# Kernel optimization log

Measured on AMD Instinct MI355X. Metric: run time of the kernel, lower is better.

Reference implementation:

```python
import jax, jax.numpy as jnp
import numpy as np

N = 100000  # nodes
E = 1600000  # edges


def gcn_conv(x, W, b, src, dst, n_nodes):
    """PyG-style GCNConv: add self-loops, symmetric norm, linear, scatter-add, bias."""
    h = x @ W  # [N, F_out]
    loop = jnp.arange(n_nodes, dtype=src.dtype)
    s = jnp.concatenate([src, loop])  # source nodes (messages flow src -> dst)
    d = jnp.concatenate([dst, loop])
    deg = jax.ops.segment_sum(jnp.ones_like(d, dtype=h.dtype), d, num_segments=n_nodes)
    dinv = jnp.where(deg > 0, jax.lax.rsqrt(deg), 0.0)
    norm = dinv[s] * dinv[d]  # [E+N]
    msgs = h[s] * norm[:, None]  # [E+N, F_out] -- dominant memory traffic
    out = jax.ops.segment_sum(msgs, d, num_segments=n_nodes)
    return out + b


def setup_inputs() -> dict:
    key = jax.random.key(0)
    k1, k2, k3, k4 = jax.random.split(key, 4)
    x = jax.random.normal(k1, (N, 128), dtype=jnp.float32)
    edge_index = jax.random.randint(k2, (2, E), 0, N, dtype=jnp.int32)
    W1 = jax.random.normal(k3, (128, 64), dtype=jnp.float32) * (1.0 / np.sqrt(128))
    b1 = jnp.zeros((64,), dtype=jnp.float32)
    W2 = jax.random.normal(k4, (64, 16), dtype=jnp.float32) * (1.0 / np.sqrt(64))
    b2 = jnp.zeros((16,), dtype=jnp.float32)
    return {"x": x, "edge_index": edge_index, "W1": W1, "b1": b1, "W2": W2, "b2": b2}


def reference(x, edge_index, W1, b1, W2, b2):
    src, dst = edge_index[0], edge_index[1]
    h = gcn_conv(x, W1, b1, src, dst, N)
    h = jax.nn.leaky_relu(h, negative_slope=0.2)
    # dropout is identity in eval mode
    h = gcn_conv(h, W2, b2, src, dst, N)
    return jax.nn.log_softmax(h, axis=-1)
```

## Files before the change

### kernel.cpp

```cpp
#include <hip/hip_runtime.h>
#include <math.h>


#define CHUNK 4096
#define BSHIFT 8
#define BMASK 255
#define CAP 4864
#define CAPP (CAP + 40)

typedef __bf16 bf16x8 __attribute__((ext_vector_type(8)));
typedef float f32x4 __attribute__((ext_vector_type(4)));

__device__ __forceinline__ unsigned f2b(float f) {
  unsigned u = __float_as_uint(f);
  return (u + 0x7FFF + ((u >> 16) & 1)) >> 16;
}

struct f2 { float x, y; };
__device__ __forceinline__ void addu(f2& a, unsigned u) {
  a.x += __uint_as_float(u << 16);
  a.y += __uint_as_float(u);
}
__device__ __forceinline__ void addu4(f2* a, uint4 g) {
  addu(a[0], g.x); addu(a[1], g.y); addu(a[2], g.z); addu(a[3], g.w);
}

__global__ void binit_kernel(int* __restrict__ gbcursor, int nbc,
                             unsigned* __restrict__ h1s, unsigned* __restrict__ t,
                             int n) {
  int b = blockIdx.x * 256 + threadIdx.x;
  if (b < nbc) gbcursor[b] = b * CAP;
  if (blockIdx.x == 0) {
    if (threadIdx.x < 32) h1s[(size_t)n * 32 + threadIdx.x] = 0u;
    else if (threadIdx.x < 40) t[(size_t)n * 8 + (threadIdx.x - 32)] = 0u;
  }
}

__global__ __launch_bounds__(256) void scatterA_kernel(const int* __restrict__ src,
                                                       const int* __restrict__ dst,
                                                       int E, int nbc,
                                                       int* __restrict__ gbcursor,
                                                       int* __restrict__ tmp) {
  __shared__ int hist[512];
  __shared__ int segcur[512];
  int tid = threadIdx.x;
  int estart = blockIdx.x * CHUNK;
  int eend = min(E, estart + CHUNK);
  hist[tid] = 0;
  hist[tid + 256] = 0;
  __syncthreads();
  for (int i = estart + tid; i < eend; i += 256)
    atomicAdd(&hist[dst[i] >> BSHIFT], 1);
  __syncthreads();
  for (int bb = tid; bb < nbc; bb += 256) {
    int c = hist[bb];
    segcur[bb] = c ? atomicAdd(&gbcursor[bb], c) : 0;
  }
  __syncthreads();
  for (int i = estart + tid; i < eend; i += 256) {
    int d = dst[i];
    int b = d >> BSHIFT;
    int pos = atomicAdd(&segcur[b], 1);
    if (pos < (b + 1) * CAP)
      tmp[pos] = (src[i] << BSHIFT) | (d & BMASK);
  }
}

__global__ __launch_bounds__(256) void degcnt_kernel(const int* __restrict__ tmp,
                                                     const int* __restrict__ gbcursor,
                                                     int* __restrict__ degs,
                                                     float* __restrict__ dinv, int n) {
  __shared__ int nh[256];
  int b = blockIdx.x, tid = threadIdx.x;
  nh[tid] = 0;
  __syncthreads();
  int base = b * CAP;
  int count = min(gbcursor[b] - base, CAP);
  for (int i = tid; i < count; i += 256) atomicAdd(&nh[tmp[base + i] & BMASK], 1);
  __syncthreads();
  int v = (b << BSHIFT) + tid;
  if (v < n) {
    degs[v] = nh[tid];
    dinv[v] = rsqrtf((float)(nh[tid] + 1));
  }
}

__global__ __launch_bounds__(256, 4) void gemm1_kernel(const float* __restrict__ x,
                                                       const float* __restrict__ W1,
                                                       const float* __restrict__ dinv,
                                                       unsigned* __restrict__ h1s, int n) {
  __shared__ unsigned lds_u[64 * 68 * 2];
  unsigned* xs = lds_u;
  unsigned* wt = lds_u + 64 * 68;
  int tid = threadIdx.x;
  int vb = blockIdx.x * 64;
  int nrows = min(64, n - vb);

  const float4* xg = (const float4*)(x + (size_t)vb * 128);
#pragma unroll
  for (int it = 0; it < 8; ++it) {
    int idx = it * 256 + tid;
    int r = idx >> 5, c2 = idx & 31;
    float4 vv = make_float4(0.f, 0.f, 0.f, 0.f);
    if (r < nrows) vv = xg[idx];
    xs[r * 68 + c2 * 2] = (f2b(vv.y) << 16) | f2b(vv.x);
    xs[r * 68 + c2 * 2 + 1] = (f2b(vv.w) << 16) | f2b(vv.z);
  }
  unsigned short* wt16 = (unsigned short*)wt;
  const float4* wg = (const float4*)W1;
#pragma unroll
  for (int it = 0; it < 8; ++it) {
    int idx = it * 256 + tid;
    int k = idx >> 4, n0 = (idx & 15) * 4;
    float4 wv = wg[idx];
    wt16[(n0 + 0) * 136 + k] = (unsigned short)f2b(wv.x);
    wt16[(n0 + 1) * 136 + k] = (unsigned short)f2b(wv.y);
    wt16[(n0 + 2) * 136 + k] = (unsigned short)f2b(wv.z);
    wt16[(n0 + 3) * 136 + k] = (unsigned short)f2b(wv.w);
  }
  __syncthreads();

  int lane = tid & 63, wid = tid >> 6;
  int m16 = lane & 15, quad = lane >> 4;
  const unsigned* xp = xs + (wid * 16 + m16) * 68 + quad * 4;
  const unsigned* wp = wt + m16 * 68 + quad * 4;
  f32x4 acc[4] = {};
#pragma unroll
  for (int ks = 0; ks < 4; ++ks) {
    bf16x8 a = *(const bf16x8*)(xp + ks * 16);
#pragma unroll
    for (int nt = 0; nt < 4; ++nt) {
      bf16x8 b = *(const bf16x8*)(wp + nt * 16 * 68 + ks * 16);
      acc[nt] = __builtin_amdgcn_mfma_f32_16x16x32_bf16(a, b, acc[nt], 0, 0, 0);
    }
  }
  int rbase = vb + wid * 16 + quad * 4;
  float dvv[4];
#pragma unroll
  for (int reg = 0; reg < 4; ++reg) {
    int row = rbase + reg;
    dvv[reg] = (row < n) ? dinv[row] : 0.f;
  }
  unsigned short* h16 = (unsigned short*)h1s;
#pragma unroll
  for (int nt = 0; nt < 4; ++nt) {
    int col = nt * 16 + m16;
#pragma unroll
    for (int reg = 0; reg < 4; ++reg) {
      int row = rbase + reg;
      if (row < n)
        h16[(size_t)row * 64 + col] = (unsigned short)f2b(dvv[reg] * acc[nt][reg]);
    }
  }
}

template <int NQ>
__device__ __forceinline__ void gatherTier1(const uint4* __restrict__ h1s4,
                                            const int* lcsr, int rs, int e1,
                                            int e, int c, int n, f2* a0) {
  int cv0[NQ], cv1[NQ];
#pragma unroll
  for (int q = 0; q < NQ; ++q) {
    cv0[q] = lcsr[rs + q * 8 + e];
    cv1[q] = lcsr[rs + q * 8 + 4 + e];
  }
  uint4 g[2 * NQ];
#pragma unroll
  for (int q = 0; q < NQ; ++q) {
    int k0 = rs + q * 8 + e, k1 = k0 + 4;
    int s0 = (k0 < e1) ? cv0[q] : n;
    int s1 = (k1 < e1) ? cv1[q] : n;
    g[2 * q] = h1s4[(size_t)s0 * 8 + c];
    g[2 * q + 1] = h1s4[(size_t)s1 * 8 + c];
  }
#pragma unroll
  for (int k = 0; k < 2 * NQ; ++k) addu4(a0, g[k]);
}

__global__ __launch_bounds__(1024) void agg1_fused_kernel(
    const int* __restrict__ tmp, const int* __restrict__ gbcursor,
    const uint4* __restrict__ h1s4, const float* __restrict__ dinv,
    const float* __restrict__ b1, const float* __restrict__ W2,
    const int* __restrict__ degs, int* __restrict__ row_start,
    int* __restrict__ csr, unsigned* __restrict__ t, int n) {
  __shared__ int lcsr[CAPP];
  __shared__ int nh[256];
  __shared__ int rs_s[256];
  __shared__ int lcur[256];
  __shared__ float W2s[64 * 17];
  __shared__ float b1s[64];
  __shared__ float a_s[16][2][64];
  int b = blockIdx.x, tid = threadIdx.x;
  int base = b * CAP;
  int count = min(gbcursor[b] - base, CAP);

  if (tid < 256) {
    int v = (b << BSHIFT) + tid;
    int d = (v < n) ? degs[v] : 0;
    nh[tid] = d;
    rs_s[tid] = d;
  }
  W2s[(tid >> 4) * 17 + (tid & 15)] = W2[tid];
  if (tid < 64) b1s[tid] = b1[tid];
  __syncthreads();
  for (int off = 1; off < 256; off <<= 1) {
    int a = 0;
    if (tid < 256) { a = rs_s[tid]; if (tid >= off) a += rs_s[tid - off]; }
    __syncthreads();
    if (tid < 256) rs_s[tid] = a;
    __syncthreads();
  }
  if (tid < 256) {
    int e0 = rs_s[tid] - nh[tid];
    lcur[tid] = e0;
    rs_s[tid] = e0;
    int v = (b << BSHIFT) + tid;
    if (v < n) row_start[v] = base + e0;
  }
  __syncthreads();
  for (int i = tid; i < count; i += 1024) {
    int val = tmp[base + i];
    int pos = atomicAdd(&lcur[val & BMASK], 1);
    lcsr[pos] = val >> BSHIFT;
  }
  __syncthreads();
  for (int i = tid; i < count; i += 1024) csr[base + i] = lcsr[i];

  int wave = tid >> 6, lane = tid & 63;
  int half = lane >> 5, sub = lane & 31;
  int e = sub >> 3, c = sub & 7;
  int j = sub & 15, grp = (sub >> 4) & 1;

#pragma unroll 1
  for (int it = 0; it < 8; ++it) {
    int nl = wave * 16 + it * 2 + half;
    int v = (b << BSHIFT) + nl;
    bool valid = (v < n);
    int rs = rs_s[nl];
    int deg = nh[nl];
    int e1 = rs + deg;
    float dv = valid ? dinv[valid ? v : 0] : 0.f;

    f2 a0[4];
#pragma unroll
    for (int k = 0; k < 4; ++k) a0[k] = {0.f, 0.f};
    {
      int s = (valid && sub < 8) ? v : n;
      addu4(a0, h1s4[(size_t)s * 8 + c]);
    }
    int dm = max(deg, __shfl_xor(deg, 32, 64));
    int start;
    if (dm <= 16) {
      gatherTier1<2>(h1s4, lcsr, rs, e1, e, c, n, a0);
      start = 16;
    } else if (dm <= 24) {
      gatherTier1<3>(h1s4, lcsr, rs, e1, e, c, n, a0);
      start = 24;
    } else {
      gatherTier1<4>(h1s4, lcsr, rs, e1, e, c, n, a0);
      start = 32;
    }
    int i = rs + start;
    while (__any(i < e1)) {
      int i0 = i + e, i1 = i + 4 + e;
      int s0v = lcsr[i0];
      int s1v = lcsr[i1];
      int s0 = (i0 < e1) ? s0v : n;
      int s1 = (i1 < e1) ? s1v : n;
      addu4(a0, h1s4[(size_t)s0 * 8 + c]);
      addu4(a0, h1s4[(size_t)s1 * 8 + c]);
      i += 8;
    }
#pragma unroll
    for (int m = 8; m <= 16; m <<= 1) {
#pragma unroll
      for (int k = 0; k < 4; ++k) {
        a0[k].x += __shfl_xor(a0[k].x, m, 64);
        a0[k].y += __shfl_xor(a0[k].y, m, 64);
      }
    }
    if (sub < 8) {
#pragma unroll
      for (int k = 0; k < 4; ++k) {
        float z0 = fmaf(dv, a0[k].x, b1s[8 * sub + 2 * k]);
        float z1 = fmaf(dv, a0[k].y, b1s[8 * sub + 2 * k + 1]);
        a_s[wave][half][8 * sub + 2 * k] = fmaxf(z0, 0.2f * z0);
        a_s[wave][half][8 * sub + 2 * k + 1] = fmaxf(z1, 0.2f * z1);
      }
    }
    float p = 0.f;
#pragma unroll
    for (int q = 0; q < 16; ++q) {
      int f = grp * 16 + q;
      p = fmaf(a_s[wave][half][f], W2s[f * 17 + j], p);
    }
#pragma unroll
    for (int q = 0; q < 16; ++q) {
      int f = 32 + grp * 16 + q;
      p = fmaf(a_s[wave][half][f], W2s[f * 17 + j], p);
    }
    p += __shfl_xor(p, 16, 64);
    float pv = dv * p;
    float po = __shfl_xor(pv, 1, 64);
    if (valid && sub < 16 && !(sub & 1))
      t[(size_t)v * 8 + (sub >> 1)] = (f2b(po) << 16) | f2b(pv);
  }
}

__global__ __launch_bounds__(256) void agg2_kernel(const uint4* __restrict__ t4,
                                                   const float* __restrict__ dinv,
                                                   const int* __restrict__ row_start,
                                                   const int* __restrict__ degs,
                                                   const int* __restrict__ csr,
                                                   const float* __restrict__ b2,
                                                   float* __restrict__ out, int n) {
  int idx = blockIdx.x * 256 + threadIdx.x;
  int v = idx >> 4;
  if (v >= n) return;
  int sub = threadIdx.x & 15;
  int e = sub >> 1, c = sub & 1;
  float dv = dinv[v];
  int rs = row_start[v], e1 = rs + degs[v];
  f2 A0[4];
#pragma unroll
  for (int k = 0; k < 4; ++k) A0[k] = {0.f, 0.f};
  {
    int s = (e == 0) ? v : n;
    addu4(A0, t4[(size_t)s * 2 + c]);
  }
  int cv[4];
#pragma unroll
  for (int q = 0; q < 4; ++q) cv[q] = csr[rs + q * 8 + e];
  uint4 g[4];
#pragma unroll
  for (int q = 0; q < 4; ++q) {
    int k = rs + q * 8 + e;
    int s = (k < e1) ? cv[q] : n;
    g[q] = t4[(size_t)s * 2 + c];
  }
#pragma unroll
  for (int k = 0; k < 4; ++k) addu4(A0, g[k]);
  int i = rs + 32;
  while (i < e1) {
    int i0 = i + e;
    int sv = csr[i0];
    int s = (i0 < e1) ? sv : n;
    addu4(A0, t4[(size_t)s * 2 + c]);
    i += 8;
  }
#pragma unroll
  for (int m = 2; m <= 8; m <<= 1) {
#pragma unroll
    for (int k = 0; k < 4; ++k) {
      A0[k].x += __shfl_xor(A0[k].x, m, 64);
      A0[k].y += __shfl_xor(A0[k].y, m, 64);
    }
  }
  float4 bb0 = ((const float4*)b2)[c * 2];
  float4 bb1 = ((const float4*)b2)[c * 2 + 1];
  float z[8];
  z[0] = fmaf(dv, A0[0].x, bb0.x); z[1] = fmaf(dv, A0[0].y, bb0.y);
  z[2] = fmaf(dv, A0[1].x, bb0.z); z[3] = fmaf(dv, A0[1].y, bb0.w);
  z[4] = fmaf(dv, A0[2].x, bb1.x); z[5] = fmaf(dv, A0[2].y, bb1.y);
  z[6] = fmaf(dv, A0[3].x, bb1.z); z[7] = fmaf(dv, A0[3].y, bb1.w);
  float mx = z[0];
#pragma unroll
  for (int q = 1; q < 8; ++q) mx = fmaxf(mx, z[q]);
  mx = fmaxf(mx, __shfl_xor(mx, 1, 64));
  float ss = 0.f;
#pragma unroll
  for (int q = 0; q < 8; ++q) ss += expf(z[q] - mx);
  ss += __shfl_xor(ss, 1, 64);
  float lg = mx + logf(ss);
  if (e == 0) {
    float4 r0 = make_float4(z[0] - lg, z[1] - lg, z[2] - lg, z[3] - lg);
    float4 r1 = make_float4(z[4] - lg, z[5] - lg, z[6] - lg, z[7] - lg);
    float4* o = (float4*)out + (size_t)v * 4 + c * 2;
    o[0] = r0;
    o[1] = r1;
  }
}

extern "C" void kernel_launch(void* const* d_in, const int* in_sizes, int n_in,
                              void* d_out, int out_size, void* d_ws, size_t ws_size,
                              hipStream_t stream) {
  const float* x = (const float*)d_in[0];
  const int* edge_index = (const int*)d_in[1];
  const float* W1 = (const float*)d_in[2];
  const float* b1 = (const float*)d_in[3];
  const float* W2 = (const float*)d_in[4];
  const float* b2 = (const float*)d_in[5];
  float* out = (float*)d_out;

  int N_ = in_sizes[0] / 128;
  int E_ = in_sizes[1] / 2;
  const int* src = edge_index;
  const int* dst = edge_index + E_;
  int NBc = (N_ + BMASK) >> BSHIFT;

  char* ws = (char*)d_ws;
  size_t off = 0;
  auto take = [&](size_t bytes) {
    void* p = ws + off;
    off += (bytes + 255) & ~(size_t)255;
    return p;
  };
  unsigned* h1s = (unsigned*)take(((size_t)N_ + 1) * 32 * 4);
  unsigned* t = (unsigned*)take(((size_t)N_ + 1) * 8 * 4);
  int* tmp = (int*)take((size_t)NBc * CAP * 4);
  int* csr = (int*)take(((size_t)NBc * CAP + 64) * 4);
  float* dinv = (float*)take((size_t)N_ * 4);
  int* degs = (int*)take((size_t)N_ * 4);
  int* row_start = (int*)take((size_t)N_ * 4);
  int* gbcursor = (int*)take((size_t)NBc * 4);
  (void)ws_size;

  binit_kernel<<<(NBc + 255) / 256, 256, 0, stream>>>(gbcursor, NBc, h1s, t, N_);
  scatterA_kernel<<<(E_ + CHUNK - 1) / CHUNK, 256, 0, stream>>>(src, dst, E_, NBc,
                                                                gbcursor, tmp);
  degcnt_kernel<<<NBc, 256, 0, stream>>>(tmp, gbcursor, degs, dinv, N_);
  gemm1_kernel<<<(N_ + 63) / 64, 256, 0, stream>>>(x, W1, dinv, h1s, N_);
  agg1_fused_kernel<<<NBc, 1024, 0, stream>>>(tmp, gbcursor, (const uint4*)h1s,
                                              dinv, b1, W2, degs, row_start, csr,
                                              t, N_);
  agg2_kernel<<<(N_ * 16 + 255) / 256, 256, 0, stream>>>((const uint4*)t, dinv,
                                                         row_start, degs, csr,
                                                         b2, out, N_);
}
```

Before: 203.4 us.

## Split layer-2 GEMM out of agg1 into separate MFMA bf16 kernel

Removes the per-node 64x16 W2 projection from the fused aggregation kernel. agg1 now writes bf16 leaky-relu activations to a new h2in buffer, and a new gemm2 kernel computes them times W2 with MFMA 16x16x32 bf16 instructions before scaling by dinv. This takes the LDS traffic and scalar FMA loop out of the latency-bound gather kernel and may improve its occupancy. The cost is an extra launch and a write plus re-read of a 64-wide bf16 intermediate of about 12.8MB, and W2 is now rounded to bf16.

New measurement: 209.6 us. +3.1%, slower.

```diff
diff --git a/kernel.cpp b/kernel.cpp
--- a/kernel.cpp
+++ b/kernel.cpp
@@ -180,16 +180,14 @@
 __global__ __launch_bounds__(1024) void agg1_fused_kernel(
     const int* __restrict__ tmp, const int* __restrict__ gbcursor,
     const uint4* __restrict__ h1s4, const float* __restrict__ dinv,
-    const float* __restrict__ b1, const float* __restrict__ W2,
-    const int* __restrict__ degs, int* __restrict__ row_start,
-    int* __restrict__ csr, unsigned* __restrict__ t, int n) {
+    const float* __restrict__ b1, const int* __restrict__ degs,
+    int* __restrict__ row_start, int* __restrict__ csr,
+    unsigned* __restrict__ h2in, int n) {
   __shared__ int lcsr[CAPP];
   __shared__ int nh[256];
   __shared__ int rs_s[256];
   __shared__ int lcur[256];
-  __shared__ float W2s[64 * 17];
   __shared__ float b1s[64];
-  __shared__ float a_s[16][2][64];
   int b = blockIdx.x, tid = threadIdx.x;
   int base = b * CAP;
   int count = min(gbcursor[b] - base, CAP);
@@ -200,7 +198,6 @@
     nh[tid] = d;
     rs_s[tid] = d;
   }
-  W2s[(tid >> 4) * 17 + (tid & 15)] = W2[tid];
   if (tid < 64) b1s[tid] = b1[tid];
   __syncthreads();
   for (int off = 1; off < 256; off <<= 1) {
@@ -229,7 +226,6 @@
   int wave = tid >> 6, lane = tid & 63;
   int half = lane >> 5, sub = lane & 31;
   int e = sub >> 3, c = sub & 7;
-  int j = sub & 15, grp = (sub >> 4) & 1;
 
 #pragma unroll 1
   for (int it = 0; it < 8; ++it) {
@@ -279,31 +275,57 @@
         a0[k].y += __shfl_xor(a0[k].y, m, 64);
       }
     }
-    if (sub < 8) {
+    if (valid && sub < 8) {
+      float z[8];
 #pragma unroll
       for (int k = 0; k < 4; ++k) {
         float z0 = fmaf(dv, a0[k].x, b1s[8 * sub + 2 * k]);
         float z1 = fmaf(dv, a0[k].y, b1s[8 * sub + 2 * k + 1]);
-        a_s[wave][half][8 * sub + 2 * k] = fmaxf(z0, 0.2f * z0);
-        a_s[wave][half][8 * sub + 2 * k + 1] = fmaxf(z1, 0.2f * z1);
+        z[2 * k] = fmaxf(z0, 0.2f * z0);
+        z[2 * k + 1] = fmaxf(z1, 0.2f * z1);
       }
-    }
-    float p = 0.f;
-#pragma unroll
-    for (int q = 0; q < 16; ++q) {
-      int f = grp * 16 + q;
-      p = fmaf(a_s[wave][half][f], W2s[f * 17 + j], p);
-    }
-#pragma unroll
-    for (int q = 0; q < 16; ++q) {
-      int f = 32 + grp * 16 + q;
-      p = fmaf(a_s[wave][half][f], W2s[f * 17 + j], p);
-    }
-    p += __shfl_xor(p, 16, 64);
-    float pv = dv * p;
-    float po = __shfl_xor(pv, 1, 64);
-    if (valid && sub < 16 && !(sub & 1))
-      t[(size_t)v * 8 + (sub >> 1)] = (f2b(po) << 16) | f2b(pv);
+      uint4 o;
+      o.x = (f2b(z[1]) << 16) | f2b(z[0]);
+      o.y = (f2b(z[3]) << 16) | f2b(z[2]);
+      o.z = (f2b(z[5]) << 16) | f2b(z[4]);
+      o.w = (f2b(z[7]) << 16) | f2b(z[6]);
+      ((uint4*)h2in)[(size_t)v * 8 + sub] = o;
+    }
+  }
+}
+
+__global__ __launch_bounds__(256) void gemm2_kernel(const uint4* __restrict__ h2in4,
+                                                    const float* __restrict__ W2,
+                                                    const float* __restrict__ dinv,
+                                                    unsigned* __restrict__ t, int n) {
+  int tid = threadIdx.x;
+  int lane = tid & 63, wid = tid >> 6;
+  int m16 = lane & 15, quad = lane >> 4;
+  union { bf16x8 v; unsigned short s[8]; } bu0, bu1;
+#pragma unroll
+  for (int j = 0; j < 8; ++j) {
+    bu0.s[j] = (unsigned short)f2b(W2[(quad * 8 + j) * 16 + m16]);
+    bu1.s[j] = (unsigned short)f2b(W2[(32 + quad * 8 + j) * 16 + m16]);
+  }
+#pragma unroll 1
+  for (int pass = 0; pass < 4; ++pass) {
+    int rt = blockIdx.x * 256 + pass * 64 + wid * 16;
+    int row_a = rt + m16;
+    int ra = (row_a < n) ? row_a : 0;
+    uint4 av0 = h2in4[(size_t)ra * 8 + quad];
+    uint4 av1 = h2in4[(size_t)ra * 8 + 4 + quad];
+    f32x4 acc = {};
+    acc = __builtin_amdgcn_mfma_f32_16x16x32_bf16(*(const bf16x8*)&av0, bu0.v, acc, 0, 0, 0);
+    acc = __builtin_amdgcn_mfma_f32_16x16x32_bf16(*(const bf16x8*)&av1, bu1.v, acc, 0, 0, 0);
+#pragma unroll
+    for (int reg = 0; reg < 4; ++reg) {
+      int row = rt + quad * 4 + reg;
+      float dv = (row < n) ? dinv[row] : 0.f;
+      float val = dv * acc[reg];
+      float other = __shfl_xor(val, 1, 64);
+      if (!(m16 & 1) && row < n)
+        t[(size_t)row * 8 + (m16 >> 1)] = (f2b(other) << 16) | f2b(val);
+    }
   }
 }
 
@@ -406,6 +428,7 @@
     return p;
   };
   unsigned* h1s = (unsigned*)take(((size_t)N_ + 1) * 32 * 4);
+  unsigned* h2in = (unsigned*)take(((size_t)N_ + 256) * 32 * 4);
   unsigned* t = (unsigned*)take(((size_t)N_ + 1) * 8 * 4);
   int* tmp = (int*)take((size_t)NBc * CAP * 4);
   int* csr = (int*)take(((size_t)NBc * CAP + 64) * 4);
@@ -421,8 +444,10 @@
   degcnt_kernel<<<NBc, 256, 0, stream>>>(tmp, gbcursor, degs, dinv, N_);
   gemm1_kernel<<<(N_ + 63) / 64, 256, 0, stream>>>(x, W1, dinv, h1s, N_);
   agg1_fused_kernel<<<NBc, 1024, 0, stream>>>(tmp, gbcursor, (const uint4*)h1s,
-                                              dinv, b1, W2, degs, row_start, csr,
-                                              t, N_);
+                                              dinv, b1, degs, row_start, csr,
+                                              h2in, N_);
+  gemm2_kernel<<<(N_ + 255) / 256, 256, 0, stream>>>((const uint4*)h2in, W2, dinv,
+                                                     t, N_);
   agg2_kernel<<<(N_ * 16 + 255) / 256, 256, 0, stream>>>((const uint4*)t, dinv,
                                                          row_start, degs, csr,
                                                          b2, out, N_);
```

## Merge edge bucketing and GEMM1 into one launch, scale h1 after degree count

Applied to the files above, without the earlier changes.

Edge bucketing and the first dense GEMM now run as two block roles inside a single kernel, so they overlap. The GEMM writes unscaled fp32 output to a workspace region that aliases csr and t, and a combined degree-count kernel applies dinv and converts to bf16. Buckets are widened from 256 to 512 nodes, which doubles per-block work in the aggregation kernel and halves the bucket count. This adds an extra fp32 round trip of h1 through memory and changes occupancy and per-bucket capacity.

Measured after the change: 204.9 us. No clear change (+0.8%).

```diff
diff --git a/kernel.cpp b/kernel.cpp
--- a/kernel.cpp
+++ b/kernel.cpp
@@ -2,10 +2,10 @@
 #include <math.h>
 
 
-#define CHUNK 4096
-#define BSHIFT 8
-#define BMASK 255
-#define CAP 4864
+#define CHUNK 8192
+#define BSHIFT 9
+#define BMASK 511
+#define CAP 9216
 #define CAPP (CAP + 40)
 
 typedef __bf16 bf16x8 __attribute__((ext_vector_type(8)));
@@ -26,130 +26,133 @@
 }
 
 __global__ void binit_kernel(int* __restrict__ gbcursor, int nbc,
-                             unsigned* __restrict__ h1s, unsigned* __restrict__ t,
-                             int n) {
+                             unsigned* __restrict__ h1s, int n) {
   int b = blockIdx.x * 256 + threadIdx.x;
   if (b < nbc) gbcursor[b] = b * CAP;
-  if (blockIdx.x == 0) {
-    if (threadIdx.x < 32) h1s[(size_t)n * 32 + threadIdx.x] = 0u;
-    else if (threadIdx.x < 40) t[(size_t)n * 8 + (threadIdx.x - 32)] = 0u;
-  }
-}
-
-__global__ __launch_bounds__(256) void scatterA_kernel(const int* __restrict__ src,
-                                                       const int* __restrict__ dst,
-                                                       int E, int nbc,
-                                                       int* __restrict__ gbcursor,
-                                                       int* __restrict__ tmp) {
-  __shared__ int hist[512];
-  __shared__ int segcur[512];
+  if (blockIdx.x == 0 && threadIdx.x < 32) h1s[(size_t)n * 32 + threadIdx.x] = 0u;
+}
+
+__global__ __launch_bounds__(256, 4) void combo_kernel(
+    const int* __restrict__ src, const int* __restrict__ dst, int E, int nbc,
+    int nSc, int* __restrict__ gbcursor, int* __restrict__ tmp,
+    const float* __restrict__ x, const float* __restrict__ W1,
+    float* __restrict__ h1u, int n) {
+  __shared__ unsigned shbuf[64 * 68 * 2];
   int tid = threadIdx.x;
-  int estart = blockIdx.x * CHUNK;
-  int eend = min(E, estart + CHUNK);
-  hist[tid] = 0;
-  hist[tid + 256] = 0;
-  __syncthreads();
-  for (int i = estart + tid; i < eend; i += 256)
-    atomicAdd(&hist[dst[i] >> BSHIFT], 1);
-  __syncthreads();
-  for (int bb = tid; bb < nbc; bb += 256) {
-    int c = hist[bb];
-    segcur[bb] = c ? atomicAdd(&gbcursor[bb], c) : 0;
-  }
-  __syncthreads();
-  for (int i = estart + tid; i < eend; i += 256) {
-    int d = dst[i];
-    int b = d >> BSHIFT;
-    int pos = atomicAdd(&segcur[b], 1);
-    if (pos < (b + 1) * CAP)
-      tmp[pos] = (src[i] << BSHIFT) | (d & BMASK);
-  }
-}
-
-__global__ __launch_bounds__(256) void degcnt_kernel(const int* __restrict__ tmp,
-                                                     const int* __restrict__ gbcursor,
-                                                     int* __restrict__ degs,
-                                                     float* __restrict__ dinv, int n) {
-  __shared__ int nh[256];
+
+  if ((int)blockIdx.x < nSc) {
+    int* hist = (int*)shbuf;
+    int* segcur = hist + 256;
+    int estart = blockIdx.x * CHUNK;
+    int eend = min(E, estart + CHUNK);
+    hist[tid] = 0;
+    __syncthreads();
+    for (int i = estart + tid; i < eend; i += 256)
+      atomicAdd(&hist[dst[i] >> BSHIFT], 1);
+    __syncthreads();
+    if (tid < nbc) {
+      int c = hist[tid];
+      segcur[tid] = c ? atomicAdd(&gbcursor[tid], c) : 0;
+    }
+    __syncthreads();
+    for (int i = estart + tid; i < eend; i += 256) {
+      int d = dst[i];
+      int b = d >> BSHIFT;
+      int pos = atomicAdd(&segcur[b], 1);
+      if (pos < (b + 1) * CAP)
+        tmp[pos] = (src[i] << BSHIFT) | (d & BMASK);
+    }
+  } else {
+    unsigned* xs = shbuf;
+    unsigned* wt = shbuf + 64 * 68;
+    int vb = ((int)blockIdx.x - nSc) * 64;
+    int nrows = min(64, n - vb);
+
+    const float4* xg = (const float4*)(x + (size_t)vb * 128);
+#pragma unroll
+    for (int it = 0; it < 8; ++it) {
+      int idx = it * 256 + tid;
+      int r = idx >> 5, c2 = idx & 31;
+      float4 vv = make_float4(0.f, 0.f, 0.f, 0.f);
+      if (r < nrows) vv = xg[idx];
+      xs[r * 68 + c2 * 2] = (f2b(vv.y) << 16) | f2b(vv.x);
+      xs[r * 68 + c2 * 2 + 1] = (f2b(vv.w) << 16) | f2b(vv.z);
+    }
+    unsigned short* wt16 = (unsigned short*)wt;
+    const float4* wg = (const float4*)W1;
+#pragma unroll
+    for (int it = 0; it < 8; ++it) {
+      int idx = it * 256 + tid;
+      int k = idx >> 4, n0 = (idx & 15) * 4;
+      float4 wv = wg[idx];
+      wt16[(n0 + 0) * 136 + k] = (unsigned short)f2b(wv.x);
+      wt16[(n0 + 1) * 136 + k] = (unsigned short)f2b(wv.y);
+      wt16[(n0 + 2) * 136 + k] = (unsigned short)f2b(wv.z);
+      wt16[(n0 + 3) * 136 + k] = (unsigned short)f2b(wv.w);
+    }
+    __syncthreads();
+
+    int lane = tid & 63, wid = tid >> 6;
+    int m16 = lane & 15, quad = lane >> 4;
+    const unsigned* xp = xs + (wid * 16 + m16) * 68 + quad * 4;
+    const unsigned* wp = wt + m16 * 68 + quad * 4;
+    f32x4 acc[4] = {};
+#pragma unroll
+    for (int ks = 0; ks < 4; ++ks) {
+      bf16x8 a = *(const bf16x8*)(xp + ks * 16);
+#pragma unroll
+      for (int nt = 0; nt < 4; ++nt) {
+        bf16x8 b = *(const bf16x8*)(wp + nt * 16 * 68 + ks * 16);
+        acc[nt] = __builtin_amdgcn_mfma_f32_16x16x32_bf16(a, b, acc[nt], 0, 0, 0);
+      }
+    }
+    int rbase = vb + wid * 16 + quad * 4;
+#pragma unroll
+    for (int nt = 0; nt < 4; ++nt) {
+      int col = nt * 16 + m16;
+#pragma unroll
+      for (int reg = 0; reg < 4; ++reg) {
+        int row = rbase + reg;
+        if (row < n) h1u[(size_t)row * 64 + col] = acc[nt][reg];
+      }
+    }
+  }
+}
+
+__global__ __launch_bounds__(512) void degcnt_scale_kernel(
+    const int* __restrict__ tmp, const int* __restrict__ gbcursor,
+    const float4* __restrict__ h1u4, int* __restrict__ degs,
+    float* __restrict__ dinv, unsigned* __restrict__ h1s, int n) {
+  __shared__ int nh[512];
+  __shared__ float dl[512];
   int b = blockIdx.x, tid = threadIdx.x;
   nh[tid] = 0;
   __syncthreads();
   int base = b * CAP;
   int count = min(gbcursor[b] - base, CAP);
-  for (int i = tid; i < count; i += 256) atomicAdd(&nh[tmp[base + i] & BMASK], 1);
-  __syncthreads();
-  int v = (b << BSHIFT) + tid;
-  if (v < n) {
-    degs[v] = nh[tid];
-    dinv[v] = rsqrtf((float)(nh[tid] + 1));
-  }
-}
-
-__global__ __launch_bounds__(256, 4) void gemm1_kernel(const float* __restrict__ x,
-                                                       const float* __restrict__ W1,
-                                                       const float* __restrict__ dinv,
-                                                       unsigned* __restrict__ h1s, int n) {
-  __shared__ unsigned lds_u[64 * 68 * 2];
-  unsigned* xs = lds_u;
-  unsigned* wt = lds_u + 64 * 68;
-  int tid = threadIdx.x;
-  int vb = blockIdx.x * 64;
-  int nrows = min(64, n - vb);
-
-  const float4* xg = (const float4*)(x + (size_t)vb * 128);
-#pragma unroll
-  for (int it = 0; it < 8; ++it) {
-    int idx = it * 256 + tid;
-    int r = idx >> 5, c2 = idx & 31;
-    float4 vv = make_float4(0.f, 0.f, 0.f, 0.f);
-    if (r < nrows) vv = xg[idx];
-    xs[r * 68 + c2 * 2] = (f2b(vv.y) << 16) | f2b(vv.x);
-    xs[r * 68 + c2 * 2 + 1] = (f2b(vv.w) << 16) | f2b(vv.z);
-  }
-  unsigned short* wt16 = (unsigned short*)wt;
-  const float4* wg = (const float4*)W1;
-#pragma unroll
-  for (int it = 0; it < 8; ++it) {
-    int idx = it * 256 + tid;
-    int k = idx >> 4, n0 = (idx & 15) * 4;
-    float4 wv = wg[idx];
-    wt16[(n0 + 0) * 136 + k] = (unsigned short)f2b(wv.x);
-    wt16[(n0 + 1) * 136 + k] = (unsigned short)f2b(wv.y);
-    wt16[(n0 + 2) * 136 + k] = (unsigned short)f2b(wv.z);
-    wt16[(n0 + 3) * 136 + k] = (unsigned short)f2b(wv.w);
-  }
-  __syncthreads();
-
-  int lane = tid & 63, wid = tid >> 6;
-  int m16 = lane & 15, quad = lane >> 4;
-  const unsigned* xp = xs + (wid * 16 + m16) * 68 + quad * 4;
-  const unsigned* wp = wt + m16 * 68 + quad * 4;
-  f32x4 acc[4] = {};
-#pragma unroll
-  for (int ks = 0; ks < 4; ++ks) {
-    bf16x8 a = *(const bf16x8*)(xp + ks * 16);
-#pragma unroll
-    for (int nt = 0; nt < 4; ++nt) {
-      bf16x8 b = *(const bf16x8*)(wp + nt * 16 * 68 + ks * 16);
-      acc[nt] = __builtin_amdgcn_mfma_f32_16x16x32_bf16(a, b, acc[nt], 0, 0, 0);
-    }
-  }
-  int rbase = vb + wid * 16 + quad * 4;
-  float dvv[4];
-#pragma unroll
-  for (int reg = 0; reg < 4; ++reg) {
-    int row = rbase + reg;
-    dvv[reg] = (row < n) ? dinv[row] : 0.f;
-  }
-  unsigned short* h16 = (unsigned short*)h1s;
-#pragma unroll
-  for (int nt = 0; nt < 4; ++nt) {
-    int col = nt * 16 + m16;
-#pragma unroll
-    for (int reg = 0; reg < 4; ++reg) {
-      int row = rbase + reg;
-      if (row < n)
-        h16[(size_t)row * 64 + col] = (unsigned short)f2b(dvv[reg] * acc[nt][reg]);
+  for (int i = tid; i < count; i += 512) atomicAdd(&nh[tmp[base + i] & BMASK], 1);
+  __syncthreads();
+  int v0 = (b << BSHIFT) + tid;
+  float dvv = rsqrtf((float)(nh[tid] + 1));
+  dl[tid] = dvv;
+  if (v0 < n) {
+    degs[v0] = nh[tid];
+    dinv[v0] = dvv;
+  }
+  __syncthreads();
+  uint2* h1s2 = (uint2*)h1s;
+#pragma unroll 4
+  for (int it = 0; it < 16; ++it) {
+    int idx = it * 512 + tid;
+    int rl = idx >> 4, q = idx & 15;
+    int v = (b << BSHIFT) + rl;
+    if (v < n) {
+      float4 vv = h1u4[(size_t)v * 16 + q];
+      float dv = dl[rl];
+      uint2 o;
+      o.x = (f2b(dv * vv.y) << 16) | f2b(dv * vv.x);
+      o.y = (f2b(dv * vv.w) << 16) | f2b(dv * vv.z);
+      h1s2[(size_t)v * 16 + q] = o;
     }
   }
 }
@@ -184,9 +187,9 @@
     const int* __restrict__ degs, int* __restrict__ row_start,
     int* __restrict__ csr, unsigned* __restrict__ t, int n) {
   __shared__ int lcsr[CAPP];
-  __shared__ int nh[256];
-  __shared__ int rs_s[256];
-  __shared__ int lcur[256];
+  __shared__ int nh[512];
+  __shared__ int rs_s[512];
+  __shared__ int lcur[512];
   __shared__ float W2s[64 * 17];
   __shared__ float b1s[64];
   __shared__ float a_s[16][2][64];
@@ -194,7 +197,7 @@
   int base = b * CAP;
   int count = min(gbcursor[b] - base, CAP);
 
-  if (tid < 256) {
+  if (tid < 512) {
     int v = (b << BSHIFT) + tid;
     int d = (v < n) ? degs[v] : 0;
     nh[tid] = d;
@@ -202,15 +205,17 @@
   }
   W2s[(tid >> 4) * 17 + (tid & 15)] = W2[tid];
   if (tid < 64) b1s[tid] = b1[tid];
-  __syncthreads();
-  for (int off = 1; off < 256; off <<= 1) {
+  if (b == 0 && tid >= 64 && tid < 72)
+    t[(size_t)n * 8 + (tid - 64)] = 0u;
+  __syncthreads();
+  for (int off = 1; off < 512; off <<= 1) {
     int a = 0;
-    if (tid < 256) { a = rs_s[tid]; if (tid >= off) a += rs_s[tid - off]; }
-    __syncthreads();
-    if (tid < 256) rs_s[tid] = a;
-    __syncthreads();
-  }
-  if (tid < 256) {
+    if (tid < 512) { a = rs_s[tid]; if (tid >= off) a += rs_s[tid - off]; }
+    __syncthreads();
+    if (tid < 512) rs_s[tid] = a;
+    __syncthreads();
+  }
+  if (tid < 512) {
     int e0 = rs_s[tid] - nh[tid];
     lcur[tid] = e0;
     rs_s[tid] = e0;
@@ -232,8 +237,8 @@
   int j = sub & 15, grp = (sub >> 4) & 1;
 
 #pragma unroll 1
-  for (int it = 0; it < 8; ++it) {
-    int nl = wave * 16 + it * 2 + half;
+  for (int it = 0; it < 16; ++it) {
+    int nl = wave * 32 + it * 2 + half;
     int v = (b << BSHIFT) + nl;
     bool valid = (v < n);
     int rs = rs_s[nl];
@@ -397,6 +402,8 @@
   const int* src = edge_index;
   const int* dst = edge_index + E_;
   int NBc = (N_ + BMASK) >> BSHIFT;
+  int nSc = (E_ + CHUNK - 1) / CHUNK;
+  int nG1 = (N_ + 63) / 64;
 
   char* ws = (char*)d_ws;
   size_t off = 0;
@@ -406,20 +413,26 @@
     return p;
   };
   unsigned* h1s = (unsigned*)take(((size_t)N_ + 1) * 32 * 4);
-  unsigned* t = (unsigned*)take(((size_t)N_ + 1) * 8 * 4);
+  size_t h1u_b = (size_t)N_ * 64 * 4;
+  size_t csr_b = (((size_t)NBc * CAP + 64) * 4 + 255) & ~(size_t)255;
+  size_t t_b = ((size_t)N_ + 1) * 8 * 4;
+  size_t A_b = h1u_b > csr_b + t_b ? h1u_b : csr_b + t_b;
+  char* A = (char*)take(A_b);
+  float* h1u = (float*)A;
+  int* csr = (int*)A;
+  unsigned* t = (unsigned*)(A + csr_b);
   int* tmp = (int*)take((size_t)NBc * CAP * 4);
-  int* csr = (int*)take(((size_t)NBc * CAP + 64) * 4);
   float* dinv = (float*)take((size_t)N_ * 4);
   int* degs = (int*)take((size_t)N_ * 4);
   int* row_start = (int*)take((size_t)N_ * 4);
   int* gbcursor = (int*)take((size_t)NBc * 4);
   (void)ws_size;
 
-  binit_kernel<<<(NBc + 255) / 256, 256, 0, stream>>>(gbcursor, NBc, h1s, t, N_);
-  scatterA_kernel<<<(E_ + CHUNK - 1) / CHUNK, 256, 0, stream>>>(src, dst, E_, NBc,
-                                                                gbcursor, tmp);
-  degcnt_kernel<<<NBc, 256, 0, stream>>>(tmp, gbcursor, degs, dinv, N_);
-  gemm1_kernel<<<(N_ + 63) / 64, 256, 0, stream>>>(x, W1, dinv, h1s, N_);
+  binit_kernel<<<(NBc + 255) / 256, 256, 0, stream>>>(gbcursor, NBc, h1s, N_);
+  combo_kernel<<<nSc + nG1, 256, 0, stream>>>(src, dst, E_, NBc, nSc, gbcursor,
+                                              tmp, x, W1, h1u, N_);
+  degcnt_scale_kernel<<<NBc, 512, 0, stream>>>(tmp, gbcursor, (const float4*)h1u,
+                                               degs, dinv, h1s, N_);
   agg1_fused_kernel<<<NBc, 1024, 0, stream>>>(tmp, gbcursor, (const uint4*)h1s,
                                               dinv, b1, W2, degs, row_start, csr,
                                               t, N_);
```

## Double node bucket size to 512 and load GEMM A-operand directly into registers

Applied to the files above, without the earlier changes.

Node buckets grow from 256 to 512 nodes, with matching capacity. The scatter, degree-count and fused aggregation kernels are resized for the larger buckets, and each aggregation wave now handles 32 nodes instead of 16. This halves the bucket count (about 196) and cuts cursor atomics and per-block overhead, but leaves fewer, heavier blocks and more LDS per block, which may hurt occupancy. Separately, gemm1 drops the LDS staging of x and has each lane read its A fragment straight from global memory into registers, removing LDS writes and a round trip at the cost of less coalesced loads.

After: 193.0 us. -5.1%, faster.

```diff
diff --git a/kernel.cpp b/kernel.cpp
--- a/kernel.cpp
+++ b/kernel.cpp
@@ -3,9 +3,9 @@
 
 
 #define CHUNK 4096
-#define BSHIFT 8
-#define BMASK 255
-#define CAP 4864
+#define BSHIFT 9
+#define BMASK 511
+#define CAP 9216
 #define CAPP (CAP + 40)
 
 typedef __bf16 bf16x8 __attribute__((ext_vector_type(8)));
@@ -41,20 +41,19 @@
                                                        int E, int nbc,
                                                        int* __restrict__ gbcursor,
                                                        int* __restrict__ tmp) {
-  __shared__ int hist[512];
-  __shared__ int segcur[512];
+  __shared__ int hist[256];
+  __shared__ int segcur[256];
   int tid = threadIdx.x;
   int estart = blockIdx.x * CHUNK;
   int eend = min(E, estart + CHUNK);
   hist[tid] = 0;
-  hist[tid + 256] = 0;
   __syncthreads();
   for (int i = estart + tid; i < eend; i += 256)
     atomicAdd(&hist[dst[i] >> BSHIFT], 1);
   __syncthreads();
-  for (int bb = tid; bb < nbc; bb += 256) {
-    int c = hist[bb];
-    segcur[bb] = c ? atomicAdd(&gbcursor[bb], c) : 0;
+  if (tid < nbc) {
+    int c = hist[tid];
+    segcur[tid] = c ? atomicAdd(&gbcursor[tid], c) : 0;
   }
   __syncthreads();
   for (int i = estart + tid; i < eend; i += 256) {
@@ -66,17 +65,17 @@
   }
 }
 
-__global__ __launch_bounds__(256) void degcnt_kernel(const int* __restrict__ tmp,
+__global__ __launch_bounds__(512) void degcnt_kernel(const int* __restrict__ tmp,
                                                      const int* __restrict__ gbcursor,
                                                      int* __restrict__ degs,
                                                      float* __restrict__ dinv, int n) {
-  __shared__ int nh[256];
+  __shared__ int nh[512];
   int b = blockIdx.x, tid = threadIdx.x;
   nh[tid] = 0;
   __syncthreads();
   int base = b * CAP;
   int count = min(gbcursor[b] - base, CAP);
-  for (int i = tid; i < count; i += 256) atomicAdd(&nh[tmp[base + i] & BMASK], 1);
+  for (int i = tid; i < count; i += 512) atomicAdd(&nh[tmp[base + i] & BMASK], 1);
   __syncthreads();
   int v = (b << BSHIFT) + tid;
   if (v < n) {
@@ -89,23 +88,10 @@
                                                        const float* __restrict__ W1,
                                                        const float* __restrict__ dinv,
                                                        unsigned* __restrict__ h1s, int n) {
-  __shared__ unsigned lds_u[64 * 68 * 2];
-  unsigned* xs = lds_u;
-  unsigned* wt = lds_u + 64 * 68;
+  __shared__ unsigned wt[64 * 68];
   int tid = threadIdx.x;
   int vb = blockIdx.x * 64;
-  int nrows = min(64, n - vb);
-
-  const float4* xg = (const float4*)(x + (size_t)vb * 128);
-#pragma unroll
-  for (int it = 0; it < 8; ++it) {
-    int idx = it * 256 + tid;
-    int r = idx >> 5, c2 = idx & 31;
-    float4 vv = make_float4(0.f, 0.f, 0.f, 0.f);
-    if (r < nrows) vv = xg[idx];
-    xs[r * 68 + c2 * 2] = (f2b(vv.y) << 16) | f2b(vv.x);
-    xs[r * 68 + c2 * 2 + 1] = (f2b(vv.w) << 16) | f2b(vv.z);
-  }
+
   unsigned short* wt16 = (unsigned short*)wt;
   const float4* wg = (const float4*)W1;
 #pragma unroll
@@ -122,12 +108,24 @@
 
   int lane = tid & 63, wid = tid >> 6;
   int m16 = lane & 15, quad = lane >> 4;
-  const unsigned* xp = xs + (wid * 16 + m16) * 68 + quad * 4;
+  int row_a = vb + wid * 16 + m16;
+  int ra = (row_a < n) ? row_a : n - 1;
+  const float4* xg = (const float4*)x + (size_t)ra * 32 + quad * 2;
+  unsigned a32[4][4];
+#pragma unroll
+  for (int ks = 0; ks < 4; ++ks) {
+    float4 v0 = xg[ks * 8];
+    float4 v1 = xg[ks * 8 + 1];
+    a32[ks][0] = (f2b(v0.y) << 16) | f2b(v0.x);
+    a32[ks][1] = (f2b(v0.w) << 16) | f2b(v0.z);
+    a32[ks][2] = (f2b(v1.y) << 16) | f2b(v1.x);
+    a32[ks][3] = (f2b(v1.w) << 16) | f2b(v1.z);
+  }
   const unsigned* wp = wt + m16 * 68 + quad * 4;
   f32x4 acc[4] = {};
 #pragma unroll
   for (int ks = 0; ks < 4; ++ks) {
-    bf16x8 a = *(const bf16x8*)(xp + ks * 16);
+    bf16x8 a = *(const bf16x8*)a32[ks];
 #pragma unroll
     for (int nt = 0; nt < 4; ++nt) {
       bf16x8 b = *(const bf16x8*)(wp + nt * 16 * 68 + ks * 16);
@@ -184,9 +182,9 @@
     const int* __restrict__ degs, int* __restrict__ row_start,
     int* __restrict__ csr, unsigned* __restrict__ t, int n) {
   __shared__ int lcsr[CAPP];
-  __shared__ int nh[256];
-  __shared__ int rs_s[256];
-  __shared__ int lcur[256];
+  __shared__ int nh[512];
+  __shared__ int rs_s[512];
+  __shared__ int lcur[512];
   __shared__ float W2s[64 * 17];
   __shared__ float b1s[64];
   __shared__ float a_s[16][2][64];
@@ -194,7 +192,7 @@
   int base = b * CAP;
   int count = min(gbcursor[b] - base, CAP);
 
-  if (tid < 256) {
+  if (tid < 512) {
     int v = (b << BSHIFT) + tid;
     int d = (v < n) ? degs[v] : 0;
     nh[tid] = d;
@@ -203,14 +201,14 @@
   W2s[(tid >> 4) * 17 + (tid & 15)] = W2[tid];
   if (tid < 64) b1s[tid] = b1[tid];
   __syncthreads();
-  for (int off = 1; off < 256; off <<= 1) {
+  for (int off = 1; off < 512; off <<= 1) {
     int a = 0;
-    if (tid < 256) { a = rs_s[tid]; if (tid >= off) a += rs_s[tid - off]; }
+    if (tid < 512) { a = rs_s[tid]; if (tid >= off) a += rs_s[tid - off]; }
     __syncthreads();
-    if (tid < 256) rs_s[tid] = a;
+    if (tid < 512) rs_s[tid] = a;
     __syncthreads();
   }
-  if (tid < 256) {
+  if (tid < 512) {
     int e0 = rs_s[tid] - nh[tid];
     lcur[tid] = e0;
     rs_s[tid] = e0;
@@ -232,8 +230,8 @@
   int j = sub & 15, grp = (sub >> 4) & 1;
 
 #pragma unroll 1
-  for (int it = 0; it < 8; ++it) {
-    int nl = wave * 16 + it * 2 + half;
+  for (int it = 0; it < 16; ++it) {
+    int nl = wave * 32 + it * 2 + half;
     int v = (b << BSHIFT) + nl;
     bool valid = (v < n);
     int rs = rs_s[nl];
@@ -418,7 +416,7 @@
   binit_kernel<<<(NBc + 255) / 256, 256, 0, stream>>>(gbcursor, NBc, h1s, t, N_);
   scatterA_kernel<<<(E_ + CHUNK - 1) / CHUNK, 256, 0, stream>>>(src, dst, E_, NBc,
                                                                 gbcursor, tmp);
-  degcnt_kernel<<<NBc, 256, 0, stream>>>(tmp, gbcursor, degs, dinv, N_);
+  degcnt_kernel<<<NBc, 512, 0, stream>>>(tmp, gbcursor, degs, dinv, N_);
   gemm1_kernel<<<(N_ + 63) / 64, 256, 0, stream>>>(x, W1, dinv, h1s, N_);
   agg1_fused_kernel<<<NBc, 1024, 0, stream>>>(tmp, gbcursor, (const uint4*)h1s,
                                               dinv, b1, W2, degs, row_start, csr,
```
